# Performance work log

Measured on AMD Instinct MI355X. Metric: run time of the kernel, lower is better.

Reference implementation:

```python
import jax, jax.numpy as jnp
import numpy as np

B = 262144
FEAT = 128
SHARED = [128, 62]   # shared trunk layer sizes (tanh)
VF = 128             # value-branch hidden size (tanh)
LATENT = 62
E = 2                # num_experts (k == E -> dense combine)
HID = 64             # expert hidden size
ACT = 6              # action_size
NOISE_EPS = 1e-2


def setup_inputs() -> dict:
    key = jax.random.key(0)
    ks = jax.random.split(key, 16)
    s = 0.02
    inp = {
        'features': jax.random.normal(ks[0], (B, FEAT), jnp.float32),
        'noise': jax.random.normal(ks[1], (B, E), jnp.float32),
        # shared trunk: 128 -> 128 -> 62, tanh
        'Ws0': s * jax.random.normal(ks[2], (FEAT, SHARED[0]), jnp.float32),
        'bs0': jnp.zeros((SHARED[0],), jnp.float32),
        'Ws1': s * jax.random.normal(ks[3], (SHARED[0], SHARED[1]), jnp.float32),
        'bs1': jnp.zeros((SHARED[1],), jnp.float32),
        # value branch: 62 -> 128, tanh
        'Wv': s * jax.random.normal(ks[4], (LATENT, VF), jnp.float32),
        'bv': jnp.zeros((VF,), jnp.float32),
        # noisy gating
        'w_gate': s * jax.random.normal(ks[5], (LATENT, E), jnp.float32),
        'w_noise': s * jax.random.normal(ks[6], (LATENT, E), jnp.float32),
        # experts: 62 -> 64 (relu) -> 6 (softmax)
        'We1': s * jax.random.normal(ks[7], (E, LATENT, HID), jnp.float32),
        'be1': jnp.zeros((E, HID), jnp.float32),
        'We2': s * jax.random.normal(ks[8], (E, HID, ACT), jnp.float32),
        'be2': jnp.zeros((E, ACT), jnp.float32),
    }
    return inp


def reference(features, noise, Ws0, bs0, Ws1, bs1, Wv, bv,
              w_gate, w_noise, We1, be1, We2, be2):
    # shared trunk
    h = jnp.tanh(features @ Ws0 + bs0)          # [B,128]
    latent = jnp.tanh(h @ Ws1 + bs1)            # [B,62]
    # value branch
    latent_vf = jnp.tanh(latent @ Wv + bv)      # [B,128]
    # noisy gating; k == num_experts so top-k softmax == full softmax
    clean_logits = latent @ w_gate              # [B,E]
    noise_std = jax.nn.softplus(latent @ w_noise) + NOISE_EPS
    noisy_logits = clean_logits + noise * noise_std
    gates = jax.nn.softmax(noisy_logits, axis=-1)  # [B,E]
    # experts (dense, vectorized over E)
    eh = jax.nn.relu(jnp.einsum('bd,edh->beh', latent, We1) + be1)  # [B,E,64]
    expout = jax.nn.softmax(jnp.einsum('beh,eho->beo', eh, We2) + be2, axis=-1)  # [B,E,6]
    action = jnp.einsum('be,beo->bo', gates, expout)  # [B,6]
    return (action, latent_vf, expout)


if __name__ == '__main__':
    out = reference(**setup_inputs())
    print([o.shape for o in out])
```

## Files before the change

kernel.cpp:

```cpp
#include <hip/hip_runtime.h>

#define BB 262144

typedef float fx4 __attribute__((ext_vector_type(4)));
typedef float fx2 __attribute__((ext_vector_type(2)));
typedef short sx8 __attribute__((ext_vector_type(8)));

__device__ unsigned short g_Wf[44032];

__device__ __forceinline__ unsigned short f2bf(float f) {
    unsigned u = __builtin_bit_cast(unsigned, f);
    u += 0x7fffu + ((u >> 16) & 1u);
    return (unsigned short)(u >> 16);
}

__device__ __forceinline__ sx8 cvt8(fx4 a, fx4 b) {
    sx8 r;
    r[0] = (short)f2bf(a[0]); r[1] = (short)f2bf(a[1]);
    r[2] = (short)f2bf(a[2]); r[3] = (short)f2bf(a[3]);
    r[4] = (short)f2bf(b[0]); r[5] = (short)f2bf(b[1]);
    r[6] = (short)f2bf(b[2]); r[7] = (short)f2bf(b[3]);
    return r;
}

__device__ __forceinline__ float fast_tanh(float x) {
    x = fminf(15.f, fmaxf(-15.f, x));
    float t = __builtin_amdgcn_exp2f(x * 2.8853900817779268f);
    return (t - 1.f) * __builtin_amdgcn_rcpf(t + 1.f);
}

__device__ __forceinline__ float fast_softplus(float x) {
    float xc = fminf(30.f, fmaxf(-30.f, x));
    float e = __builtin_amdgcn_exp2f(xc * 1.4426950408889634f);
    return 0.6931471805599453f * __builtin_amdgcn_logf(1.f + e);
}

__global__ void pack_all(const float* __restrict__ Ws0, const float* __restrict__ Ws1,
                         const float* __restrict__ Wv,  const float* __restrict__ wg,
                         const float* __restrict__ wn,  const float* __restrict__ We1,
                         const float* __restrict__ We2)
{
    int idx = blockIdx.x * 256 + threadIdx.x;
    int off, KT, mode, Ksrc = 0, Nsrc = 0;
    const float* src; const float* src2 = nullptr;
    if (idx < 16384)      { off = 0;     KT = 4; mode = 0; src = Ws0; Ksrc = 128; Nsrc = 128; }
    else if (idx < 24576) { off = 16384; KT = 4; mode = 0; src = Ws1; Ksrc = 128; Nsrc = 62;  }
    else if (idx < 32768) { off = 24576; KT = 2; mode = 0; src = Wv;  Ksrc = 62;  Nsrc = 128; }
    else if (idx < 40960) { off = 32768; KT = 2; mode = 1; src = We1; }
    else if (idx < 43008) { off = 40960; KT = 4; mode = 2; src = We2; }
    else                  { off = 43008; KT = 2; mode = 3; src = wg; src2 = wn; }

    int rel  = idx - off;
    int blk  = rel >> 9;
    int lane = (rel >> 3) & 63;
    int j    = rel & 7;
    int nt = blk / KT, kt = blk - nt * KT;
    int k = kt * 32 + (lane >> 4) * 8 + j;
    int n = nt * 16 + (lane & 15);
    float v = 0.f;
    if (mode == 0) {
        if (k < Ksrc && n < Nsrc) v = src[k * Nsrc + n];
    } else if (mode == 1) {
        if (k < 62) { int e = n >> 6, h = n & 63; v = src[e * 3968 + k * 64 + h]; }
    } else if (mode == 2) {
        int e = k >> 6; int c = n - e * 6;
        if ((unsigned)c < 6u) v = src[e * 384 + (k & 63) * 6 + c];
    } else {
        if (k < 62) {
            if (n < 2) v = src[k * 2 + n];
            else if (n < 4) v = src2[k * 2 + (n - 2)];
        }
    }
    g_Wf[idx] = f2bf(v);
}

__global__ __launch_bounds__(256, 2)
void mlp_main(const float* __restrict__ X, const float* __restrict__ noise,
              const float* __restrict__ bs0, const float* __restrict__ bs1,
              const float* __restrict__ bv,  const float* __restrict__ be1,
              const float* __restrict__ be2, float* __restrict__ out)
{
    __shared__ __align__(16) unsigned short sH[128 * 136];
    __shared__ __align__(16) unsigned short sL[128 * 72];
    __shared__ __align__(16) float sS[128 * 21];

    const int tid  = threadIdx.x;
    const int wave = tid >> 6;
    const int lane = tid & 63;
    const int lr   = lane & 15;
    const int lq   = lane >> 4;
    const int r0   = blockIdx.x * 128;

    const unsigned short* W0f  = g_Wf;
    const unsigned short* W1f  = g_Wf + 16384;
    const unsigned short* Wvf  = g_Wf + 24576;
    const unsigned short* We1f = g_Wf + 32768;
    const unsigned short* W2f  = g_Wf + 40960;
    const unsigned short* Wgf  = g_Wf + 43008;

    float* out_act = out;
    float* out_vf  = out + (size_t)6 * BB;
    float* out_eo  = out + (size_t)134 * BB;

    sx8 a[2][4];
    for (int m = 0; m < 2; m++) {
        const float* p = X + (size_t)(r0 + (wave * 2 + m) * 16 + lr) * 128 + lq * 8;
        for (int kt = 0; kt < 4; kt++) {
            fx4 u = *(const fx4*)(p + kt * 32);
            fx4 v = *(const fx4*)(p + kt * 32 + 4);
            a[m][kt] = cvt8(u, v);
        }
    }
    for (int nt = 0; nt < 8; nt++) {
        sx8 b[4];
        for (int kt = 0; kt < 4; kt++)
            b[kt] = *(const sx8*)(W0f + (((nt * 4 + kt) * 64 + lane) << 3));
        int col = nt * 16 + lr;
        float bias = bs0[col];
        for (int m = 0; m < 2; m++) {
            fx4 acc = {0.f, 0.f, 0.f, 0.f};
            for (int kt = 0; kt < 4; kt++)
                acc = __builtin_amdgcn_mfma_f32_16x16x32_bf16(a[m][kt], b[kt], acc, 0, 0, 0);
            unsigned short* dst = sH + ((wave * 2 + m) * 16 + lq * 4) * 136 + col;
            for (int r = 0; r < 4; r++)
                dst[r * 136] = f2bf(fast_tanh(acc[r] + bias));
        }
    }
    __syncthreads();

    for (int m = 0; m < 2; m++)
        for (int kt = 0; kt < 4; kt++)
            a[m][kt] = *(const sx8*)(sH + ((wave * 2 + m) * 16 + lr) * 136 + kt * 32 + lq * 8);
    for (int nt = 0; nt < 4; nt++) {
        sx8 b[4];
        for (int kt = 0; kt < 4; kt++)
            b[kt] = *(const sx8*)(W1f + (((nt * 4 + kt) * 64 + lane) << 3));
        int col = nt * 16 + lr;
        float bias = (col < 62) ? bs1[col] : 0.f;
        for (int m = 0; m < 2; m++) {
            fx4 acc = {0.f, 0.f, 0.f, 0.f};
            for (int kt = 0; kt < 4; kt++)
                acc = __builtin_amdgcn_mfma_f32_16x16x32_bf16(a[m][kt], b[kt], acc, 0, 0, 0);
            unsigned short* dst = sL + ((wave * 2 + m) * 16 + lq * 4) * 72 + col;
            for (int r = 0; r < 4; r++)
                dst[r * 72] = f2bf(fast_tanh(acc[r] + bias));
        }
    }
    __syncthreads();

    sx8 aL[2][2];
    for (int m = 0; m < 2; m++)
        for (int kt = 0; kt < 2; kt++)
            aL[m][kt] = *(const sx8*)(sL + ((wave * 2 + m) * 16 + lr) * 72 + kt * 32 + lq * 8);
    for (int nt = 0; nt < 8; nt++) {
        sx8 b0 = *(const sx8*)(We1f + (((nt * 2 + 0) * 64 + lane) << 3));
        sx8 b1 = *(const sx8*)(We1f + (((nt * 2 + 1) * 64 + lane) << 3));
        int col = nt * 16 + lr;
        float bias = be1[col];
        for (int m = 0; m < 2; m++) {
            fx4 acc = {0.f, 0.f, 0.f, 0.f};
            acc = __builtin_amdgcn_mfma_f32_16x16x32_bf16(aL[m][0], b0, acc, 0, 0, 0);
            acc = __builtin_amdgcn_mfma_f32_16x16x32_bf16(aL[m][1], b1, acc, 0, 0, 0);
            unsigned short* dst = sH + ((wave * 2 + m) * 16 + lq * 4) * 136 + col;
            for (int r = 0; r < 4; r++)
                dst[r * 136] = f2bf(fmaxf(acc[r] + bias, 0.f));
        }
    }
    for (int nt = 0; nt < 8; nt++) {
        sx8 b0 = *(const sx8*)(Wvf + (((nt * 2 + 0) * 64 + lane) << 3));
        sx8 b1 = *(const sx8*)(Wvf + (((nt * 2 + 1) * 64 + lane) << 3));
        int col = nt * 16 + lr;
        float bias = bv[col];
        for (int m = 0; m < 2; m++) {
            fx4 acc = {0.f, 0.f, 0.f, 0.f};
            acc = __builtin_amdgcn_mfma_f32_16x16x32_bf16(aL[m][0], b0, acc, 0, 0, 0);
            acc = __builtin_amdgcn_mfma_f32_16x16x32_bf16(aL[m][1], b1, acc, 0, 0, 0);
            float* dst = out_vf + (size_t)(r0 + (wave * 2 + m) * 16 + lq * 4) * 128 + col;
            for (int r = 0; r < 4; r++)
                dst[(size_t)r * 128] = fast_tanh(acc[r] + bias);
        }
    }
    __syncthreads();

    {
        sx8 bw[4];
        for (int kt = 0; kt < 4; kt++)
            bw[kt] = *(const sx8*)(W2f + (((kt) * 64 + lane) << 3));
        for (int m = 0; m < 2; m++) {
            sx8 ae[4];
            for (int kt = 0; kt < 4; kt++)
                ae[kt] = *(const sx8*)(sH + ((wave * 2 + m) * 16 + lr) * 136 + kt * 32 + lq * 8);
            fx4 acc = {0.f, 0.f, 0.f, 0.f};
            for (int kt = 0; kt < 4; kt++)
                acc = __builtin_amdgcn_mfma_f32_16x16x32_bf16(ae[kt], bw[kt], acc, 0, 0, 0);
            float* dst = sS + ((wave * 2 + m) * 16 + lq * 4) * 21 + lr;
            for (int r = 0; r < 4; r++) dst[r * 21] = acc[r];
        }
    }
    {
        sx8 bg0 = *(const sx8*)(Wgf + ((0 * 64 + lane) << 3));
        sx8 bg1 = *(const sx8*)(Wgf + ((1 * 64 + lane) << 3));
        for (int m = 0; m < 2; m++) {
            fx4 acc = {0.f, 0.f, 0.f, 0.f};
            acc = __builtin_amdgcn_mfma_f32_16x16x32_bf16(aL[m][0], bg0, acc, 0, 0, 0);
            acc = __builtin_amdgcn_mfma_f32_16x16x32_bf16(aL[m][1], bg1, acc, 0, 0, 0);
            if (lr < 4) {
                float* dst = sS + ((wave * 2 + m) * 16 + lq * 4) * 21 + 16 + lr;
                for (int r = 0; r < 4; r++) dst[r * 21] = acc[r];
            }
        }
    }
    __syncthreads();

    if (tid < 128) {
        const float* Srow = sS + tid * 21;
        int grow = r0 + tid;
        fx2 nz = *(const fx2*)(noise + (size_t)grow * 2);
        float sp0 = fast_softplus(Srow[18]) + 1e-2f;
        float sp1 = fast_softplus(Srow[19]) + 1e-2f;
        float l0 = Srow[16] + nz[0] * sp0;
        float l1 = Srow[17] + nz[1] * sp1;
        float mg = fmaxf(l0, l1);
        float e0 = __builtin_amdgcn_exp2f((l0 - mg) * 1.4426950408889634f);
        float e1 = __builtin_amdgcn_exp2f((l1 - mg) * 1.4426950408889634f);
        float gi = __builtin_amdgcn_rcpf(e0 + e1);
        float g0 = e0 * gi, g1 = e1 * gi;

        float eo[12];
        for (int e = 0; e < 2; e++) {
            float lg[6]; float mx = -1e30f;
            for (int c = 0; c < 6; c++) {
                lg[c] = Srow[e * 6 + c] + be2[e * 6 + c];
                mx = fmaxf(mx, lg[c]);
            }
            float s = 0.f;
            for (int c = 0; c < 6; c++) {
                lg[c] = __builtin_amdgcn_exp2f((lg[c] - mx) * 1.4426950408889634f);
                s += lg[c];
            }
            float inv = __builtin_amdgcn_rcpf(s);
            for (int c = 0; c < 6; c++) eo[e * 6 + c] = lg[c] * inv;
        }
        float* pa = out_act + (size_t)grow * 6;
        for (int c = 0; c < 6; c++) pa[c] = g0 * eo[c] + g1 * eo[6 + c];
        float* pe = out_eo + (size_t)grow * 12;
        for (int c = 0; c < 12; c++) pe[c] = eo[c];
    }
}

extern "C" void kernel_launch(void* const* d_in, const int* in_sizes, int n_in,
                              void* d_out, int out_size, void* d_ws, size_t ws_size,
                              hipStream_t stream)
{
    const float* X    = (const float*)d_in[0];
    const float* nz   = (const float*)d_in[1];
    const float* Ws0  = (const float*)d_in[2];
    const float* bs0  = (const float*)d_in[3];
    const float* Ws1  = (const float*)d_in[4];
    const float* bs1  = (const float*)d_in[5];
    const float* Wv   = (const float*)d_in[6];
    const float* bv   = (const float*)d_in[7];
    const float* wg   = (const float*)d_in[8];
    const float* wn   = (const float*)d_in[9];
    const float* We1  = (const float*)d_in[10];
    const float* be1  = (const float*)d_in[11];
    const float* We2  = (const float*)d_in[12];
    const float* be2  = (const float*)d_in[13];

    pack_all<<<172, 256, 0, stream>>>(Ws0, Ws1, Wv, wg, wn, We1, We2);

    mlp_main<<<BB / 128, 256, 0, stream>>>(X, nz, bs0, bs1, bv, be1, be2, (float*)d_out);
}
```

Baseline: 304.2 us.

## Make shared-memory staging per-wave, drop block barriers, raise occupancy

Each wave now owns a private 8.7KB LDS slice that is reused across all stages, so the block-wide __syncthreads are replaced with wave barriers. LDS per block shrinks enough that launch bounds can rise to 4 blocks per CU. The final softmax and gating epilogue now runs on all four waves (32 lanes each) instead of two, and the outputs are written with vector stores. The bf16 packing is also done in pairs. The risks are that wave_barrier ordering alone might not guarantee LDS visibility, and the higher occupancy target may cause register spills.

Measured after the change: 307.6 us. Within noise of the previous version (+1.1%).

```diff
diff --git a/kernel.cpp b/kernel.cpp
--- a/kernel.cpp
+++ b/kernel.cpp
@@ -5,6 +5,13 @@
 typedef float fx4 __attribute__((ext_vector_type(4)));
 typedef float fx2 __attribute__((ext_vector_type(2)));
 typedef short sx8 __attribute__((ext_vector_type(8)));
+typedef unsigned ux4 __attribute__((ext_vector_type(4)));
+
+#if __has_builtin(__builtin_amdgcn_wave_barrier)
+#define WB() __builtin_amdgcn_wave_barrier()
+#else
+#define WB()
+#endif
 
 __device__ unsigned short g_Wf[44032];
 
@@ -14,13 +21,15 @@
     return (unsigned short)(u >> 16);
 }
 
+__device__ __forceinline__ unsigned pk2(float x, float y) {
+    return (unsigned)f2bf(x) | ((unsigned)f2bf(y) << 16);
+}
+
 __device__ __forceinline__ sx8 cvt8(fx4 a, fx4 b) {
-    sx8 r;
-    r[0] = (short)f2bf(a[0]); r[1] = (short)f2bf(a[1]);
-    r[2] = (short)f2bf(a[2]); r[3] = (short)f2bf(a[3]);
-    r[4] = (short)f2bf(b[0]); r[5] = (short)f2bf(b[1]);
-    r[6] = (short)f2bf(b[2]); r[7] = (short)f2bf(b[3]);
-    return r;
+    ux4 u;
+    u[0] = pk2(a[0], a[1]); u[1] = pk2(a[2], a[3]);
+    u[2] = pk2(b[0], b[1]); u[3] = pk2(b[2], b[3]);
+    return __builtin_bit_cast(sx8, u);
 }
 
 __device__ __forceinline__ float fast_tanh(float x) {
@@ -74,22 +83,23 @@
     g_Wf[idx] = f2bf(v);
 }
 
-__global__ __launch_bounds__(256, 2)
+__global__ __launch_bounds__(256, 4)
 void mlp_main(const float* __restrict__ X, const float* __restrict__ noise,
               const float* __restrict__ bs0, const float* __restrict__ bs1,
               const float* __restrict__ bv,  const float* __restrict__ be1,
               const float* __restrict__ be2, float* __restrict__ out)
 {
-    __shared__ __align__(16) unsigned short sH[128 * 136];
-    __shared__ __align__(16) unsigned short sL[128 * 72];
-    __shared__ __align__(16) float sS[128 * 21];
+    __shared__ __align__(16) unsigned short smem[4 * 4352];
 
     const int tid  = threadIdx.x;
     const int wave = tid >> 6;
     const int lane = tid & 63;
     const int lr   = lane & 15;
     const int lq   = lane >> 4;
-    const int r0   = blockIdx.x * 128;
+    const int wr0  = blockIdx.x * 128 + wave * 32;
+
+    unsigned short* sW  = smem + wave * 4352;
+    float*          sSf = (float*)sW;
 
     const unsigned short* W0f  = g_Wf;
     const unsigned short* W1f  = g_Wf + 16384;
@@ -104,7 +114,7 @@
 
     sx8 a[2][4];
     for (int m = 0; m < 2; m++) {
-        const float* p = X + (size_t)(r0 + (wave * 2 + m) * 16 + lr) * 128 + lq * 8;
+        const float* p = X + (size_t)(wr0 + m * 16 + lr) * 128 + lq * 8;
         for (int kt = 0; kt < 4; kt++) {
             fx4 u = *(const fx4*)(p + kt * 32);
             fx4 v = *(const fx4*)(p + kt * 32 + 4);
@@ -121,16 +131,17 @@
             fx4 acc = {0.f, 0.f, 0.f, 0.f};
             for (int kt = 0; kt < 4; kt++)
                 acc = __builtin_amdgcn_mfma_f32_16x16x32_bf16(a[m][kt], b[kt], acc, 0, 0, 0);
-            unsigned short* dst = sH + ((wave * 2 + m) * 16 + lq * 4) * 136 + col;
+            unsigned short* dst = sW + (m * 16 + lq * 4) * 136 + col;
             for (int r = 0; r < 4; r++)
                 dst[r * 136] = f2bf(fast_tanh(acc[r] + bias));
         }
     }
-    __syncthreads();
+    WB();
 
     for (int m = 0; m < 2; m++)
         for (int kt = 0; kt < 4; kt++)
-            a[m][kt] = *(const sx8*)(sH + ((wave * 2 + m) * 16 + lr) * 136 + kt * 32 + lq * 8);
+            a[m][kt] = *(const sx8*)(sW + (m * 16 + lr) * 136 + kt * 32 + lq * 8);
+    WB();
     for (int nt = 0; nt < 4; nt++) {
         sx8 b[4];
         for (int kt = 0; kt < 4; kt++)
@@ -141,17 +152,18 @@
             fx4 acc = {0.f, 0.f, 0.f, 0.f};
             for (int kt = 0; kt < 4; kt++)
                 acc = __builtin_amdgcn_mfma_f32_16x16x32_bf16(a[m][kt], b[kt], acc, 0, 0, 0);
-            unsigned short* dst = sL + ((wave * 2 + m) * 16 + lq * 4) * 72 + col;
+            unsigned short* dst = sW + (m * 16 + lq * 4) * 72 + col;
             for (int r = 0; r < 4; r++)
                 dst[r * 72] = f2bf(fast_tanh(acc[r] + bias));
         }
     }
-    __syncthreads();
+    WB();
 
     sx8 aL[2][2];
     for (int m = 0; m < 2; m++)
         for (int kt = 0; kt < 2; kt++)
-            aL[m][kt] = *(const sx8*)(sL + ((wave * 2 + m) * 16 + lr) * 72 + kt * 32 + lq * 8);
+            aL[m][kt] = *(const sx8*)(sW + (m * 16 + lr) * 72 + kt * 32 + lq * 8);
+    WB();
     for (int nt = 0; nt < 8; nt++) {
         sx8 b0 = *(const sx8*)(We1f + (((nt * 2 + 0) * 64 + lane) << 3));
         sx8 b1 = *(const sx8*)(We1f + (((nt * 2 + 1) * 64 + lane) << 3));
@@ -161,7 +173,7 @@
             fx4 acc = {0.f, 0.f, 0.f, 0.f};
             acc = __builtin_amdgcn_mfma_f32_16x16x32_bf16(aL[m][0], b0, acc, 0, 0, 0);
             acc = __builtin_amdgcn_mfma_f32_16x16x32_bf16(aL[m][1], b1, acc, 0, 0, 0);
-            unsigned short* dst = sH + ((wave * 2 + m) * 16 + lq * 4) * 136 + col;
+            unsigned short* dst = sW + (m * 16 + lq * 4) * 136 + col;
             for (int r = 0; r < 4; r++)
                 dst[r * 136] = f2bf(fmaxf(acc[r] + bias, 0.f));
         }
@@ -175,25 +187,27 @@
             fx4 acc = {0.f, 0.f, 0.f, 0.f};
             acc = __builtin_amdgcn_mfma_f32_16x16x32_bf16(aL[m][0], b0, acc, 0, 0, 0);
             acc = __builtin_amdgcn_mfma_f32_16x16x32_bf16(aL[m][1], b1, acc, 0, 0, 0);
-            float* dst = out_vf + (size_t)(r0 + (wave * 2 + m) * 16 + lq * 4) * 128 + col;
+            float* dst = out_vf + (size_t)(wr0 + m * 16 + lq * 4) * 128 + col;
             for (int r = 0; r < 4; r++)
                 dst[(size_t)r * 128] = fast_tanh(acc[r] + bias);
         }
     }
-    __syncthreads();
-
+    WB();
+
+    sx8 ae[2][4];
+    for (int m = 0; m < 2; m++)
+        for (int kt = 0; kt < 4; kt++)
+            ae[m][kt] = *(const sx8*)(sW + (m * 16 + lr) * 136 + kt * 32 + lq * 8);
+    WB();
     {
         sx8 bw[4];
         for (int kt = 0; kt < 4; kt++)
-            bw[kt] = *(const sx8*)(W2f + (((kt) * 64 + lane) << 3));
-        for (int m = 0; m < 2; m++) {
-            sx8 ae[4];
+            bw[kt] = *(const sx8*)(W2f + ((kt * 64 + lane) << 3));
+        for (int m = 0; m < 2; m++) {
+            fx4 acc = {0.f, 0.f, 0.f, 0.f};
             for (int kt = 0; kt < 4; kt++)
-                ae[kt] = *(const sx8*)(sH + ((wave * 2 + m) * 16 + lr) * 136 + kt * 32 + lq * 8);
-            fx4 acc = {0.f, 0.f, 0.f, 0.f};
-            for (int kt = 0; kt < 4; kt++)
-                acc = __builtin_amdgcn_mfma_f32_16x16x32_bf16(ae[kt], bw[kt], acc, 0, 0, 0);
-            float* dst = sS + ((wave * 2 + m) * 16 + lq * 4) * 21 + lr;
+                acc = __builtin_amdgcn_mfma_f32_16x16x32_bf16(ae[m][kt], bw[kt], acc, 0, 0, 0);
+            float* dst = sSf + (m * 16 + lq * 4) * 21 + lr;
             for (int r = 0; r < 4; r++) dst[r * 21] = acc[r];
         }
     }
@@ -205,16 +219,16 @@
             acc = __builtin_amdgcn_mfma_f32_16x16x32_bf16(aL[m][0], bg0, acc, 0, 0, 0);
             acc = __builtin_amdgcn_mfma_f32_16x16x32_bf16(aL[m][1], bg1, acc, 0, 0, 0);
             if (lr < 4) {
-                float* dst = sS + ((wave * 2 + m) * 16 + lq * 4) * 21 + 16 + lr;
+                float* dst = sSf + (m * 16 + lq * 4) * 21 + 16 + lr;
                 for (int r = 0; r < 4; r++) dst[r * 21] = acc[r];
             }
         }
     }
-    __syncthreads();
-
-    if (tid < 128) {
-        const float* Srow = sS + tid * 21;
-        int grow = r0 + tid;
+    WB();
+
+    if (lane < 32) {
+        const float* Srow = sSf + lane * 21;
+        int grow = wr0 + lane;
         fx2 nz = *(const fx2*)(noise + (size_t)grow * 2);
         float sp0 = fast_softplus(Srow[18]) + 1e-2f;
         float sp1 = fast_softplus(Srow[19]) + 1e-2f;
@@ -241,10 +255,15 @@
             float inv = __builtin_amdgcn_rcpf(s);
             for (int c = 0; c < 6; c++) eo[e * 6 + c] = lg[c] * inv;
         }
+        float* pe = out_eo + (size_t)grow * 12;
+        for (int c = 0; c < 3; c++)
+            ((fx4*)pe)[c] = *(const fx4*)(eo + 4 * c);
         float* pa = out_act + (size_t)grow * 6;
-        for (int c = 0; c < 6; c++) pa[c] = g0 * eo[c] + g1 * eo[6 + c];
-        float* pe = out_eo + (size_t)grow * 12;
-        for (int c = 0; c < 12; c++) pe[c] = eo[c];
+        for (int c = 0; c < 6; c += 2) {
+            fx2 v; v[0] = g0 * eo[c] + g1 * eo[6 + c];
+            v[1] = g0 * eo[c + 1] + g1 * eo[7 + c];
+            *(fx2*)(pa + c) = v;
+        }
     }
 }
 
@@ -268,6 +287,5 @@
     const float* be2  = (const float*)d_in[13];
 
     pack_all<<<172, 256, 0, stream>>>(Ws0, Ws1, Wv, wg, wn, We1, We2);
-
     mlp_main<<<BB / 128, 256, 0, stream>>>(X, nz, bs0, bs1, bv, be1, be2, (float*)d_out);
 }
```
